# Kernel tuning notes

Measured on AMD Instinct MI355X. Metric: run time of the kernel, lower is better.

The kernel has to match this reference:

```python
import jax, jax.numpy as jnp
import numpy as np
from jax import lax

PATCH = 16
TAU = 0.5
EPS = 1e-8  # torch CosineSimilarity default eps


def setup_inputs() -> dict:
    key = jax.random.key(0)
    k1, k2, k3, k4, k5 = jax.random.split(key, 5)
    B, C, HW = 64, 3, 384
    hidden, latent = 768, 1024
    return {
        "x": jax.random.normal(k1, (B, C, HW, HW), dtype=jnp.float32),
        "conv_w": jax.random.normal(k2, (hidden, C, PATCH, PATCH), dtype=jnp.float32) * 0.02,
        "conv_b": jax.random.normal(k3, (hidden,), dtype=jnp.float32) * 0.02,
        "latent1": jax.random.normal(k4, (1, latent, hidden), dtype=jnp.float32),
        "latent2": jax.random.normal(k5, (1, latent, hidden), dtype=jnp.float32),
    }


def _cosine_scores(p, p_norm, lat):
    # p: (B, N, D); lat: (L, D) -> (B, N, L) cosine similarity
    l_norm = jnp.linalg.norm(lat, axis=-1)  # (L,)
    dots = jnp.einsum('bnd,ld->bnl', p, lat)
    denom = jnp.maximum(p_norm[:, :, None] * l_norm[None, None, :], EPS)
    return dots / denom


def reference(x, conv_w, conv_b, latent1, latent2):
    # Patch embedding: Conv2d(kernel=stride=16, padding=0)
    patch = lax.conv_general_dilated(
        x, conv_w, window_strides=(PATCH, PATCH), padding='VALID',
        dimension_numbers=('NCHW', 'OIHW', 'NCHW'))
    patch = patch + conv_b[None, :, None, None]  # (B, D, H', W')
    B, D = patch.shape[0], patch.shape[1]
    p = patch.reshape(B, D, -1).transpose(0, 2, 1)  # (B, N, D)
    p_norm = jnp.linalg.norm(p, axis=-1)  # (B, N)

    far = _cosine_scores(p, p_norm, latent1[0])    # (B, N, L)
    close = _cosine_scores(p, p_norm, latent2[0])  # (B, N, L)

    sum_close = jnp.sum(jnp.exp(close / TAU), axis=(1, 2))  # (B,)
    sum_far = jnp.sum(jnp.exp(far / TAU), axis=(1, 2))      # (B,)
    loss = -jnp.log(sum_close / sum_far)
    return loss.mean()
```

## Files before the change

### kernel.cpp

```cpp
#include <hip/hip_runtime.h>
#include <math.h>

using f32x4  = __attribute__((ext_vector_type(4))) float;
using bf16x8 = __attribute__((ext_vector_type(8))) short;

typedef const __attribute__((address_space(1))) void gas_void;
typedef __attribute__((address_space(3))) void las_void;

__device__ __forceinline__ void gl16(const void* g, void* l) {
    __builtin_amdgcn_global_load_lds((gas_void*)g, (las_void*)l, 16, 0, 0);
}

__device__ __forceinline__ unsigned short f2bf(float f) {
    union { float f; unsigned u; } v; v.f = f;
    unsigned r = v.u + 0x7fffu + ((v.u >> 16) & 1u);
    return (unsigned short)(r >> 16);
}
__device__ __forceinline__ float bf2f(unsigned short u) {
    return __uint_as_float(((unsigned)u) << 16);
}

#define VW6() asm volatile("s_waitcnt vmcnt(6)")
#define VW0() asm volatile("s_waitcnt vmcnt(0)")
#define BAR() __builtin_amdgcn_s_barrier()

__global__ void pcl_prep_x(const float* __restrict__ x, unsigned short* __restrict__ xp) {
    int t = threadIdx.x;
    int wv = t >> 6, l = t & 63;
    int p = blockIdx.x * 4 + wv;
    int b = p / 576, n = p % 576;
    int ph = n / 24, pw = n % 24;
    const float* base = x + ((size_t)(b * 3)) * 147456 + (ph * 16) * 384 + pw * 16;
    unsigned* dst = (unsigned*)(xp + (size_t)p * 768);
#pragma unroll
    for (int q = 0; q < 6; ++q) {
        int k = q * 128 + l * 2;
        int c = k >> 8, i = (k >> 4) & 15, j = k & 15;
        const float* s = base + (size_t)c * 147456 + i * 384 + j;
        float2 v = *(const float2*)s;
        unsigned lo = f2bf(v.x), hi = f2bf(v.y);
        dst[q * 64 + l] = lo | (hi << 16);
    }
}

__global__ void pcl_prep_wl(const float* __restrict__ w,
                            const float* __restrict__ l1, const float* __restrict__ l2,
                            unsigned short* __restrict__ wsW,
                            unsigned short* __restrict__ wsL) {
    int r = blockIdx.x, t = threadIdx.x;
    if (r < 768) {
        const float* src = w + (size_t)r * 768;
        unsigned short* dst = wsW + (size_t)r * 768;
#pragma unroll
        for (int i = 0; i < 12; ++i) dst[t + 64 * i] = f2bf(src[t + 64 * i]);
    } else {
        int lr = r - 768;
        const float* src = (lr < 1024) ? l1 + (size_t)lr * 768 : l2 + (size_t)(lr - 1024) * 768;
        unsigned short* dst = wsL + (size_t)lr * 768;
        float vals[12];
        float s = 0.f;
#pragma unroll
        for (int i = 0; i < 12; ++i) {
            float f = bf2f(f2bf(src[t + 64 * i]));
            vals[i] = f; s += f * f;
        }
#pragma unroll
        for (int off = 32; off; off >>= 1) s += __shfl_xor(s, off, 64);
        float rn = 1.0f / sqrtf(s);
#pragma unroll
        for (int i = 0; i < 12; ++i) dst[t + 64 * i] = f2bf(vals[i] * rn);
    }
}

#define K1_LDS 116736

__global__ __launch_bounds__(1024, 4)
void pcl_k1(const unsigned short* __restrict__ xp,
            const unsigned short* __restrict__ wsW,
            const float* __restrict__ bias,
            unsigned short* __restrict__ pbuf,
            float* __restrict__ rpn) {
    extern __shared__ char smem[];
    char* A0 = smem; char* A1 = smem + 8192; char* BB = smem + 16384;
    float* nrm = (float*)(smem + 114688);
    const int t = threadIdx.x, w = t >> 6, l = t & 63;
    const int wm = w >> 3, wn = w & 7;
    const size_t Mb = (size_t)blockIdx.x * 64;
    const int ir = l >> 3, s2 = (l & 7) ^ ir;
    const int lm = l & 15, lg4 = l >> 4;

    f32x4 acc[2][6];
#pragma unroll
    for (int m = 0; m < 2; ++m)
#pragma unroll
        for (int nf = 0; nf < 6; ++nf) acc[m][nf] = (f32x4)0.f;

    if (w < 8) gl16(xp + (Mb + w * 8 + ir) * 768 + s2 * 8, A0 + w * 1024);

    for (int kc = 0; kc < 12; ++kc) {
        __syncthreads();
#pragma unroll
        for (int rep = 0; rep < 6; ++rep) {
            int c2 = w * 6 + rep;
            gl16(wsW + (size_t)(c2 * 8 + ir) * 768 + kc * 64 + s2 * 8, BB + c2 * 1024);
        }
        if (kc < 11 && w < 8)
            gl16(xp + (Mb + w * 8 + ir) * 768 + (kc + 1) * 64 + s2 * 8,
                 ((kc & 1) ? A0 : A1) + w * 1024);
        __syncthreads();

        const char* A = (kc & 1) ? A1 : A0;
        bf16x8 a[2][2];
#pragma unroll
        for (int m = 0; m < 2; ++m)
#pragma unroll
            for (int ks = 0; ks < 2; ++ks) {
                int r = wm * 32 + m * 16 + lm, slot = ks * 4 + lg4;
                a[m][ks] = *(const bf16x8*)(A + r * 128 + ((slot ^ (r & 7)) << 4));
            }
#pragma unroll
        for (int nf = 0; nf < 6; ++nf) {
            int rb = wn * 96 + nf * 16 + lm;
#pragma unroll
            for (int ks = 0; ks < 2; ++ks) {
                int slot = ks * 4 + lg4;
                bf16x8 bb = *(const bf16x8*)(BB + rb * 128 + ((slot ^ (rb & 7)) << 4));
#pragma unroll
                for (int m = 0; m < 2; ++m)
                    acc[m][nf] = __builtin_amdgcn_mfma_f32_16x16x32_bf16(a[m][ks], bb, acc[m][nf], 0, 0, 0);
            }
        }
    }

    float rs[2][4];
#pragma unroll
    for (int m = 0; m < 2; ++m)
#pragma unroll
        for (int j = 0; j < 4; ++j) rs[m][j] = 0.f;
#pragma unroll
    for (int nf = 0; nf < 6; ++nf) {
        int d = wn * 96 + nf * 16 + lm;
        float bv = bias[d];
#pragma unroll
        for (int m = 0; m < 2; ++m)
#pragma unroll
            for (int j = 0; j < 4; ++j) {
                int r = wm * 32 + m * 16 + lg4 * 4 + j;
                unsigned short h = f2bf(acc[m][nf][j] + bv);
                pbuf[(Mb + r) * 768 + d] = h;
                float fv = bf2f(h);
                rs[m][j] += fv * fv;
            }
    }
#pragma unroll
    for (int m = 0; m < 2; ++m)
#pragma unroll
        for (int j = 0; j < 4; ++j) {
            rs[m][j] += __shfl_xor(rs[m][j], 1);
            rs[m][j] += __shfl_xor(rs[m][j], 2);
            rs[m][j] += __shfl_xor(rs[m][j], 4);
            rs[m][j] += __shfl_xor(rs[m][j], 8);
        }
    if (lm == 0) {
#pragma unroll
        for (int m = 0; m < 2; ++m)
#pragma unroll
            for (int j = 0; j < 4; ++j)
                nrm[(wm * 32 + m * 16 + lg4 * 4 + j) * 8 + wn] = rs[m][j];
    }
    __syncthreads();
    if (t < 64) {
        float s = 0.f;
#pragma unroll
        for (int i = 0; i < 8; ++i) s += nrm[t * 8 + i];
        rpn[Mb + t] = 1.0f / sqrtf(s);
    }
}

#define K2_LDS 81920

__global__ __launch_bounds__(256, 2)
void pcl_k2(const unsigned short* __restrict__ pbuf,
            const unsigned short* __restrict__ wsL,
            const float* __restrict__ rpn,
            double* __restrict__ partials) {
    extern __shared__ char smem[];
    const int t = threadIdx.x, w = t >> 6, l = t & 63;
    const int wg = (blockIdx.x & 7) * 384 + (blockIdx.x >> 3);
    const int mt = wg >> 4, nt = wg & 15;
    const size_t Mb = (size_t)mt * 192;
    const int Nb = nt * 128;
    const int wm = w >> 1, wn = w & 1;
    const int ir = l >> 3, s2 = (l & 7) ^ ir;
    const int lm = l & 15, lg4 = l >> 4;

    char* buf0 = smem;
    char* buf1 = smem + 40960;

    auto issueA = [&](int kt, char* buf) {
#pragma unroll
        for (int rr = 0; rr < 6; ++rr) {
            int c2 = w * 6 + rr;
            gl16(pbuf + (Mb + c2 * 8 + ir) * 768 + kt * 64 + s2 * 8, buf + c2 * 1024);
        }
    };
    auto issueB = [&](int kt, int rep0, char* buf) {
#pragma unroll
        for (int rr = 0; rr < 2; ++rr) {
            int c2 = w * 4 + rep0 + rr;
            gl16(wsL + (size_t)(Nb + c2 * 8 + ir) * 768 + kt * 64 + s2 * 8,
                 buf + 24576 + c2 * 1024);
        }
    };

    f32x4 acc[6][4];
#pragma unroll
    for (int m = 0; m < 6; ++m)
#pragma unroll
        for (int nb = 0; nb < 4; ++nb) acc[m][nb] = (f32x4)0.f;

    issueA(0, buf0); issueB(0, 0, buf0); issueB(0, 2, buf0);
    issueA(1, buf1);
    VW6(); BAR();

    bf16x8 areg[3][2], breg[4][2];

#pragma unroll 2
    for (int kt = 0; kt < 12; ++kt) {
        char* cur = (kt & 1) ? buf1 : buf0;
        char* nxt = (kt & 1) ? buf0 : buf1;

#pragma unroll
        for (int m = 0; m < 3; ++m)
#pragma unroll
            for (int ks = 0; ks < 2; ++ks) {
                int r = wm * 96 + m * 16 + lm, slot = ks * 4 + lg4;
                areg[m][ks] = *(const bf16x8*)(cur + r * 128 + ((slot ^ (r & 7)) << 4));
            }
#pragma unroll
        for (int nb = 0; nb < 2; ++nb)
#pragma unroll
            for (int ks = 0; ks < 2; ++ks) {
                int rb = wn * 64 + nb * 16 + lm, slot = ks * 4 + lg4;
                breg[nb][ks] = *(const bf16x8*)(cur + 24576 + rb * 128 + ((slot ^ (rb & 7)) << 4));
            }
        if (kt < 11) issueB(kt + 1, 0, nxt);
        BAR();
        __builtin_amdgcn_s_setprio(1);
#pragma unroll
        for (int m = 0; m < 3; ++m)
#pragma unroll
            for (int nb = 0; nb < 2; ++nb)
#pragma unroll
                for (int ks = 0; ks < 2; ++ks)
                    acc[m][nb] = __builtin_amdgcn_mfma_f32_16x16x32_bf16(areg[m][ks], breg[nb][ks], acc[m][nb], 0, 0, 0);
        __builtin_amdgcn_s_setprio(0);
        BAR();

#pragma unroll
        for (int nb = 2; nb < 4; ++nb)
#pragma unroll
            for (int ks = 0; ks < 2; ++ks) {
                int rb = wn * 64 + nb * 16 + lm, slot = ks * 4 + lg4;
                breg[nb][ks] = *(const bf16x8*)(cur + 24576 + rb * 128 + ((slot ^ (rb & 7)) << 4));
            }
        if (kt < 11) issueB(kt + 1, 2, nxt);
        BAR();
        __builtin_amdgcn_s_setprio(1);
#pragma unroll
        for (int m = 0; m < 3; ++m)
#pragma unroll
            for (int nb = 2; nb < 4; ++nb)
#pragma unroll
                for (int ks = 0; ks < 2; ++ks)
                    acc[m][nb] = __builtin_amdgcn_mfma_f32_16x16x32_bf16(areg[m][ks], breg[nb][ks], acc[m][nb], 0, 0, 0);
        __builtin_amdgcn_s_setprio(0);
        BAR();

#pragma unroll
        for (int m = 0; m < 3; ++m)
#pragma unroll
            for (int ks = 0; ks < 2; ++ks) {
                int r = wm * 96 + 48 + m * 16 + lm, slot = ks * 4 + lg4;
                areg[m][ks] = *(const bf16x8*)(cur + r * 128 + ((slot ^ (r & 7)) << 4));
            }
        BAR();
        __builtin_amdgcn_s_setprio(1);
#pragma unroll
        for (int m = 0; m < 3; ++m)
#pragma unroll
            for (int nb = 2; nb < 4; ++nb)
#pragma unroll
                for (int ks = 0; ks < 2; ++ks)
                    acc[3 + m][nb] = __builtin_amdgcn_mfma_f32_16x16x32_bf16(areg[m][ks], breg[nb][ks], acc[3 + m][nb], 0, 0, 0);
        __builtin_amdgcn_s_setprio(0);
        BAR();

        if (kt < 10) issueA(kt + 2, cur);
        __builtin_amdgcn_s_setprio(1);
#pragma unroll
        for (int m = 0; m < 3; ++m)
#pragma unroll
            for (int nb = 0; nb < 2; ++nb)
#pragma unroll
                for (int ks = 0; ks < 2; ++ks)
                    acc[3 + m][nb] = __builtin_amdgcn_mfma_f32_16x16x32_bf16(areg[m][ks], breg[nb][ks], acc[3 + m][nb], 0, 0, 0);
        __builtin_amdgcn_s_setprio(0);
        if (kt < 10) { VW6(); } else { VW0(); }
        BAR();
    }

    double ssum = 0.0;
#pragma unroll
    for (int m = 0; m < 6; ++m) {
        int mh = m / 3, mi = m % 3;
        int rl = wm * 96 + mh * 48 + mi * 16;
        float rv[4];
#pragma unroll
        for (int j = 0; j < 4; ++j) rv[j] = rpn[Mb + rl + lg4 * 4 + j];
        float es = 0.f;
#pragma unroll
        for (int nb = 0; nb < 4; ++nb)
#pragma unroll
            for (int j = 0; j < 4; ++j)
                es += __expf(2.0f * acc[m][nb][j] * rv[j]);
        ssum += (double)es;
    }
#pragma unroll
    for (int off = 32; off; off >>= 1) ssum += __shfl_down(ssum, off);
    __syncthreads();
    double* red = (double*)smem;
    if (l == 0) red[w] = ssum;
    __syncthreads();
    if (t == 0) {
        double s = 0.0;
#pragma unroll
        for (int i = 0; i < 4; ++i) s += red[i];
        partials[wg] = s;
    }
}

__global__ void pcl_finish(const double* __restrict__ partials, float* __restrict__ out) {
    int b = threadIdx.x;
    double far = 0.0, close = 0.0;
#pragma unroll
    for (int i = 0; i < 3; ++i) {
        int mt = b * 3 + i;
#pragma unroll
        for (int nTile = 0; nTile < 16; ++nTile) {
            double v = partials[mt * 16 + nTile];
            if (nTile < 8) far += v; else close += v;
        }
    }
    double lb = log(far) - log(close);
#pragma unroll
    for (int off = 32; off; off >>= 1) lb += __shfl_down(lb, off);
    if (b == 0) out[0] = (float)(lb * (1.0 / 64.0));
}

extern "C" void kernel_launch(void* const* d_in, const int* in_sizes, int n_in,
                              void* d_out, int out_size, void* d_ws, size_t ws_size,
                              hipStream_t stream) {
    const float* x    = (const float*)d_in[0];
    const float* w    = (const float*)d_in[1];
    const float* bias = (const float*)d_in[2];
    const float* l1   = (const float*)d_in[3];
    const float* l2   = (const float*)d_in[4];
    float* out = (float*)d_out;

    unsigned short* xp  = (unsigned short*)d_ws;
    unsigned short* wsW = (unsigned short*)((char*)d_ws + 56623104);
    unsigned short* wsL = (unsigned short*)((char*)d_ws + 57802752);
    float* rpn          = (float*)((char*)d_ws + 60948480);
    double* partials    = (double*)((char*)d_ws + 61095936);

    (void)hipFuncSetAttribute((const void*)pcl_k1,
                              hipFuncAttributeMaxDynamicSharedMemorySize, K1_LDS);
    (void)hipFuncSetAttribute((const void*)pcl_k2,
                              hipFuncAttributeMaxDynamicSharedMemorySize, K2_LDS);

    pcl_prep_x<<<9216, 256, 0, stream>>>(x, xp);
    pcl_prep_wl<<<2816, 64, 0, stream>>>(w, l1, l2, wsW, wsL);
    pcl_k1<<<576, 1024, K1_LDS, stream>>>(xp, wsW, bias, xp, rpn);
    pcl_k2<<<3072, 256, K2_LDS, stream>>>(xp, wsL, rpn, partials);
    pcl_finish<<<1, 64, 0, stream>>>(partials, out);
}
```

Baseline: 232.9 us.

## Fuse patch extraction into conv GEMM and simplify score GEMM pipeline

Removes the separate pcl_prep_x kernel. The conv GEMM now loads fp32 image patches straight from x into registers one k-chunk ahead, converts them to bf16 and writes them into a single swizzled LDS A tile. This avoids writing and re-reading the 56 MB bf16 im2col buffer. The conv kernel moves to 512-thread blocks where each wave covers all 64 rows and a 96-column slice, which doubles per-wave accumulators. The score GEMM replaces its split A/B issue schedule with one prefetch per k-tile and a full vmcnt(0) wait each iteration, using fewer barriers but allowing less load/compute overlap.

```diff
diff --git a/kernel.cpp b/kernel.cpp
--- a/kernel.cpp
+++ b/kernel.cpp
@@ -20,28 +20,8 @@
     return __uint_as_float(((unsigned)u) << 16);
 }
 
-#define VW6() asm volatile("s_waitcnt vmcnt(6)")
 #define VW0() asm volatile("s_waitcnt vmcnt(0)")
 #define BAR() __builtin_amdgcn_s_barrier()
-
-__global__ void pcl_prep_x(const float* __restrict__ x, unsigned short* __restrict__ xp) {
-    int t = threadIdx.x;
-    int wv = t >> 6, l = t & 63;
-    int p = blockIdx.x * 4 + wv;
-    int b = p / 576, n = p % 576;
-    int ph = n / 24, pw = n % 24;
-    const float* base = x + ((size_t)(b * 3)) * 147456 + (ph * 16) * 384 + pw * 16;
-    unsigned* dst = (unsigned*)(xp + (size_t)p * 768);
-#pragma unroll
-    for (int q = 0; q < 6; ++q) {
-        int k = q * 128 + l * 2;
-        int c = k >> 8, i = (k >> 4) & 15, j = k & 15;
-        const float* s = base + (size_t)c * 147456 + i * 384 + j;
-        float2 v = *(const float2*)s;
-        unsigned lo = f2bf(v.x), hi = f2bf(v.y);
-        dst[q * 64 + l] = lo | (hi << 16);
-    }
-}
 
 __global__ void pcl_prep_wl(const float* __restrict__ w,
                             const float* __restrict__ l1, const float* __restrict__ l2,
@@ -72,80 +52,105 @@
     }
 }
 
-#define K1_LDS 116736
-
-__global__ __launch_bounds__(1024, 4)
-void pcl_k1(const unsigned short* __restrict__ xp,
+#define K1_LDS 108544
+
+__global__ __launch_bounds__(512, 1)
+void pcl_k1(const float* __restrict__ x,
             const unsigned short* __restrict__ wsW,
             const float* __restrict__ bias,
             unsigned short* __restrict__ pbuf,
             float* __restrict__ rpn) {
     extern __shared__ char smem[];
-    char* A0 = smem; char* A1 = smem + 8192; char* BB = smem + 16384;
-    float* nrm = (float*)(smem + 114688);
+    char* AA = smem;
+    char* BB = smem + 8192;
+    float* nrm = (float*)(smem + 106496);
     const int t = threadIdx.x, w = t >> 6, l = t & 63;
-    const int wm = w >> 3, wn = w & 7;
     const size_t Mb = (size_t)blockIdx.x * 64;
     const int ir = l >> 3, s2 = (l & 7) ^ ir;
     const int lm = l & 15, lg4 = l >> 4;
 
-    f32x4 acc[2][6];
-#pragma unroll
-    for (int m = 0; m < 2; ++m)
+    const int sr = t >> 3, ss = t & 7;
+    {
+    }
+    const int n = (int)Mb + sr;
+    const int bb_ = n / 576, n5 = n % 576;
+    const int ph = n5 / 24, pw = n5 % 24;
+    const float* xbase = x + ((size_t)(bb_ * 3)) * 147456
+                       + (size_t)(ph * 16 + (ss >> 1)) * 384 + pw * 16 + (ss & 1) * 8;
+    char* aw = AA + sr * 128 + ((ss ^ (sr & 7)) << 4);
+
+    f32x4 acc[4][6];
+#pragma unroll
+    for (int m = 0; m < 4; ++m)
 #pragma unroll
         for (int nf = 0; nf < 6; ++nf) acc[m][nf] = (f32x4)0.f;
 
-    if (w < 8) gl16(xp + (Mb + w * 8 + ir) * 768 + s2 * 8, A0 + w * 1024);
+    f32x4 xr0, xr1;
+    {
+        const float* s = xbase;
+        xr0 = *(const f32x4*)s; xr1 = *(const f32x4*)(s + 4);
+    }
 
     for (int kc = 0; kc < 12; ++kc) {
         __syncthreads();
 #pragma unroll
-        for (int rep = 0; rep < 6; ++rep) {
-            int c2 = w * 6 + rep;
+        for (int rep = 0; rep < 12; ++rep) {
+            int c2 = w + 8 * rep;
             gl16(wsW + (size_t)(c2 * 8 + ir) * 768 + kc * 64 + s2 * 8, BB + c2 * 1024);
         }
-        if (kc < 11 && w < 8)
-            gl16(xp + (Mb + w * 8 + ir) * 768 + (kc + 1) * 64 + s2 * 8,
-                 ((kc & 1) ? A0 : A1) + w * 1024);
+        {
+            bf16x8 pkt;
+#pragma unroll
+            for (int j = 0; j < 4; ++j) {
+                pkt[j]     = (short)f2bf(xr0[j]);
+                pkt[4 + j] = (short)f2bf(xr1[j]);
+            }
+            *(bf16x8*)aw = pkt;
+        }
         __syncthreads();
 
-        const char* A = (kc & 1) ? A1 : A0;
-        bf16x8 a[2][2];
-#pragma unroll
-        for (int m = 0; m < 2; ++m)
-#pragma unroll
-            for (int ks = 0; ks < 2; ++ks) {
-                int r = wm * 32 + m * 16 + lm, slot = ks * 4 + lg4;
-                a[m][ks] = *(const bf16x8*)(A + r * 128 + ((slot ^ (r & 7)) << 4));
+        if (kc < 11) {
+            int kn = kc + 1;
+            const float* s = xbase + (size_t)(kn >> 2) * 147456 + (kn & 3) * 1536;
+            xr0 = *(const f32x4*)s; xr1 = *(const f32x4*)(s + 4);
+        }
+
+        bf16x8 a[4][2];
+#pragma unroll
+        for (int m = 0; m < 4; ++m)
+#pragma unroll
+            for (int ks = 0; ks < 2; ++ks) {
+                int r = m * 16 + lm, slot = ks * 4 + lg4;
+                a[m][ks] = *(const bf16x8*)(AA + r * 128 + ((slot ^ (r & 7)) << 4));
             }
 #pragma unroll
         for (int nf = 0; nf < 6; ++nf) {
-            int rb = wn * 96 + nf * 16 + lm;
+            int rb = w * 96 + nf * 16 + lm;
 #pragma unroll
             for (int ks = 0; ks < 2; ++ks) {
                 int slot = ks * 4 + lg4;
                 bf16x8 bb = *(const bf16x8*)(BB + rb * 128 + ((slot ^ (rb & 7)) << 4));
 #pragma unroll
-                for (int m = 0; m < 2; ++m)
+                for (int m = 0; m < 4; ++m)
                     acc[m][nf] = __builtin_amdgcn_mfma_f32_16x16x32_bf16(a[m][ks], bb, acc[m][nf], 0, 0, 0);
             }
         }
     }
 
-    float rs[2][4];
-#pragma unroll
-    for (int m = 0; m < 2; ++m)
+    float rs[4][4];
+#pragma unroll
+    for (int m = 0; m < 4; ++m)
 #pragma unroll
         for (int j = 0; j < 4; ++j) rs[m][j] = 0.f;
 #pragma unroll
     for (int nf = 0; nf < 6; ++nf) {
-        int d = wn * 96 + nf * 16 + lm;
+        int d = w * 96 + nf * 16 + lm;
         float bv = bias[d];
 #pragma unroll
-        for (int m = 0; m < 2; ++m)
+        for (int m = 0; m < 4; ++m)
 #pragma unroll
             for (int j = 0; j < 4; ++j) {
-                int r = wm * 32 + m * 16 + lg4 * 4 + j;
+                int r = m * 16 + lg4 * 4 + j;
                 unsigned short h = f2bf(acc[m][nf][j] + bv);
                 pbuf[(Mb + r) * 768 + d] = h;
                 float fv = bf2f(h);
@@ -153,7 +158,7 @@
             }
     }
 #pragma unroll
-    for (int m = 0; m < 2; ++m)
+    for (int m = 0; m < 4; ++m)
 #pragma unroll
         for (int j = 0; j < 4; ++j) {
             rs[m][j] += __shfl_xor(rs[m][j], 1);
@@ -163,10 +168,10 @@
         }
     if (lm == 0) {
 #pragma unroll
-        for (int m = 0; m < 2; ++m)
+        for (int m = 0; m < 4; ++m)
 #pragma unroll
             for (int j = 0; j < 4; ++j)
-                nrm[(wm * 32 + m * 16 + lg4 * 4 + j) * 8 + wn] = rs[m][j];
+                nrm[(m * 16 + lg4 * 4 + j) * 8 + w] = rs[m][j];
     }
     __syncthreads();
     if (t < 64) {
@@ -197,17 +202,15 @@
     char* buf0 = smem;
     char* buf1 = smem + 40960;
 
-    auto issueA = [&](int kt, char* buf) {
+    auto stage = [&](int kt, char* buf) {
 #pragma unroll
         for (int rr = 0; rr < 6; ++rr) {
             int c2 = w * 6 + rr;
             gl16(pbuf + (Mb + c2 * 8 + ir) * 768 + kt * 64 + s2 * 8, buf + c2 * 1024);
         }
-    };
-    auto issueB = [&](int kt, int rep0, char* buf) {
-#pragma unroll
-        for (int rr = 0; rr < 2; ++rr) {
-            int c2 = w * 4 + rep0 + rr;
+#pragma unroll
+        for (int rr = 0; rr < 4; ++rr) {
+            int c2 = w * 4 + rr;
             gl16(wsL + (size_t)(Nb + c2 * 8 + ir) * 768 + kt * 64 + s2 * 8,
                  buf + 24576 + c2 * 1024);
         }
@@ -219,9 +222,8 @@
 #pragma unroll
         for (int nb = 0; nb < 4; ++nb) acc[m][nb] = (f32x4)0.f;
 
-    issueA(0, buf0); issueB(0, 0, buf0); issueB(0, 2, buf0);
-    issueA(1, buf1);
-    VW6(); BAR();
+    stage(0, buf0);
+    VW0(); BAR();
 
     bf16x8 areg[3][2], breg[4][2];
 
@@ -230,6 +232,15 @@
         char* cur = (kt & 1) ? buf1 : buf0;
         char* nxt = (kt & 1) ? buf0 : buf1;
 
+        if (kt < 11) stage(kt + 1, nxt);
+
+#pragma unroll
+        for (int nb = 0; nb < 4; ++nb)
+#pragma unroll
+            for (int ks = 0; ks < 2; ++ks) {
+                int rb = wn * 64 + nb * 16 + lm, slot = ks * 4 + lg4;
+                breg[nb][ks] = *(const bf16x8*)(cur + 24576 + rb * 128 + ((slot ^ (rb & 7)) << 4));
+            }
 #pragma unroll
         for (int m = 0; m < 3; ++m)
 #pragma unroll
@@ -237,45 +248,15 @@
                 int r = wm * 96 + m * 16 + lm, slot = ks * 4 + lg4;
                 areg[m][ks] = *(const bf16x8*)(cur + r * 128 + ((slot ^ (r & 7)) << 4));
             }
-#pragma unroll
-        for (int nb = 0; nb < 2; ++nb)
-#pragma unroll
-            for (int ks = 0; ks < 2; ++ks) {
-                int rb = wn * 64 + nb * 16 + lm, slot = ks * 4 + lg4;
-                breg[nb][ks] = *(const bf16x8*)(cur + 24576 + rb * 128 + ((slot ^ (rb & 7)) << 4));
-            }
-        if (kt < 11) issueB(kt + 1, 0, nxt);
-        BAR();
         __builtin_amdgcn_s_setprio(1);
 #pragma unroll
         for (int m = 0; m < 3; ++m)
 #pragma unroll
-            for (int nb = 0; nb < 2; ++nb)
+            for (int nb = 0; nb < 4; ++nb)
 #pragma unroll
                 for (int ks = 0; ks < 2; ++ks)
                     acc[m][nb] = __builtin_amdgcn_mfma_f32_16x16x32_bf16(areg[m][ks], breg[nb][ks], acc[m][nb], 0, 0, 0);
         __builtin_amdgcn_s_setprio(0);
-        BAR();
-
-#pragma unroll
-        for (int nb = 2; nb < 4; ++nb)
-#pragma unroll
-            for (int ks = 0; ks < 2; ++ks) {
-                int rb = wn * 64 + nb * 16 + lm, slot = ks * 4 + lg4;
-                breg[nb][ks] = *(const bf16x8*)(cur + 24576 + rb * 128 + ((slot ^ (rb & 7)) << 4));
-            }
-        if (kt < 11) issueB(kt + 1, 2, nxt);
-        BAR();
-        __builtin_amdgcn_s_setprio(1);
-#pragma unroll
-        for (int m = 0; m < 3; ++m)
-#pragma unroll
-            for (int nb = 2; nb < 4; ++nb)
-#pragma unroll
-                for (int ks = 0; ks < 2; ++ks)
-                    acc[m][nb] = __builtin_amdgcn_mfma_f32_16x16x32_bf16(areg[m][ks], breg[nb][ks], acc[m][nb], 0, 0, 0);
-        __builtin_amdgcn_s_setprio(0);
-        BAR();
 
 #pragma unroll
         for (int m = 0; m < 3; ++m)
@@ -284,29 +265,17 @@
                 int r = wm * 96 + 48 + m * 16 + lm, slot = ks * 4 + lg4;
                 areg[m][ks] = *(const bf16x8*)(cur + r * 128 + ((slot ^ (r & 7)) << 4));
             }
-        BAR();
         __builtin_amdgcn_s_setprio(1);
 #pragma unroll
         for (int m = 0; m < 3; ++m)
 #pragma unroll
-            for (int nb = 2; nb < 4; ++nb)
+            for (int nb = 0; nb < 4; ++nb)
 #pragma unroll
                 for (int ks = 0; ks < 2; ++ks)
                     acc[3 + m][nb] = __builtin_amdgcn_mfma_f32_16x16x32_bf16(areg[m][ks], breg[nb][ks], acc[3 + m][nb], 0, 0, 0);
         __builtin_amdgcn_s_setprio(0);
-        BAR();
-
-        if (kt < 10) issueA(kt + 2, cur);
-        __builtin_amdgcn_s_setprio(1);
-#pragma unroll
-        for (int m = 0; m < 3; ++m)
-#pragma unroll
-            for (int nb = 0; nb < 2; ++nb)
-#pragma unroll
-                for (int ks = 0; ks < 2; ++ks)
-                    acc[3 + m][nb] = __builtin_amdgcn_mfma_f32_16x16x32_bf16(areg[m][ks], breg[nb][ks], acc[3 + m][nb], 0, 0, 0);
-        __builtin_amdgcn_s_setprio(0);
-        if (kt < 10) { VW6(); } else { VW0(); }
+
+        VW0();
         BAR();
     }
 
@@ -368,20 +337,19 @@
     const float* l2   = (const float*)d_in[4];
     float* out = (float*)d_out;
 
-    unsigned short* xp  = (unsigned short*)d_ws;
-    unsigned short* wsW = (unsigned short*)((char*)d_ws + 56623104);
-    unsigned short* wsL = (unsigned short*)((char*)d_ws + 57802752);
-    float* rpn          = (float*)((char*)d_ws + 60948480);
-    double* partials    = (double*)((char*)d_ws + 61095936);
+    unsigned short* pbuf = (unsigned short*)d_ws;
+    unsigned short* wsW  = (unsigned short*)((char*)d_ws + 56623104);
+    unsigned short* wsL  = (unsigned short*)((char*)d_ws + 57802752);
+    float* rpn           = (float*)((char*)d_ws + 60948480);
+    double* partials     = (double*)((char*)d_ws + 61095936);
 
     (void)hipFuncSetAttribute((const void*)pcl_k1,
                               hipFuncAttributeMaxDynamicSharedMemorySize, K1_LDS);
     (void)hipFuncSetAttribute((const void*)pcl_k2,
                               hipFuncAttributeMaxDynamicSharedMemorySize, K2_LDS);
 
-    pcl_prep_x<<<9216, 256, 0, stream>>>(x, xp);
     pcl_prep_wl<<<2816, 64, 0, stream>>>(w, l1, l2, wsW, wsL);
-    pcl_k1<<<576, 1024, K1_LDS, stream>>>(xp, wsW, bias, xp, rpn);
-    pcl_k2<<<3072, 256, K2_LDS, stream>>>(xp, wsL, rpn, partials);
+    pcl_k1<<<576, 512, K1_LDS, stream>>>(x, wsW, bias, pbuf, rpn);
+    pcl_k2<<<3072, 256, K2_LDS, stream>>>(pbuf, wsL, rpn, partials);
     pcl_finish<<<1, 64, 0, stream>>>(partials, out);
 }
```

Result: faster. 216.8 us (-6.9%).
